# Kernel tuning notes

Hardware: AMD Instinct MI355X
Metric: run time of the kernel (lower is better)

The kernel has to match this reference:

```python
import jax, jax.numpy as jnp
import numpy as np

B, T, L = 16, 2048, 512
CH, H_ENC, H_DEC, ATTN_SZ, VOCAB, EMB = 256, 100, 200, 50, 6, 64


def _conv1d(x, k):
    # x: [B,T,Cin], k: [K,Cin,Cout], SAME padding, stride 1
    return jax.lax.conv_general_dilated(x, k, (1,), 'SAME', dimension_numbers=('NWC', 'WIO', 'NWC'))


def _lstm_step(x, c, h, W, b):
    # TF BasicLSTMCell: gates ordered [i, j, f, o], forget_bias = 1.0
    z = jnp.concatenate([x, h], -1) @ W + b
    i, j, f, o = jnp.split(z, 4, -1)
    nc = c * jax.nn.sigmoid(f + 1.0) + jax.nn.sigmoid(i) * jnp.tanh(j)
    nh = jnp.tanh(nc) * jax.nn.sigmoid(o)
    return nc, nh


def _run_lstm(xs, lengths, W, b, hidden):
    # dynamic_rnn semantics: beyond sequence_length, state held, output zeroed
    Bn, Tn, _ = xs.shape
    mask = (jnp.arange(Tn)[:, None] < lengths[None, :])[..., None]  # [T,B,1]

    def step(carry, inp):
        c, h = carry
        x, m = inp
        nc, nh = _lstm_step(x, c, h, W, b)
        c = jnp.where(m, nc, c)
        h = jnp.where(m, nh, h)
        return (c, h), jnp.where(m, nh, 0.0)

    init = (jnp.zeros((Bn, hidden), xs.dtype), jnp.zeros((Bn, hidden), xs.dtype))
    (c, h), outs = jax.lax.scan(step, init, (jnp.swapaxes(xs, 0, 1), mask))
    return jnp.swapaxes(outs, 0, 1), c, h


def _reverse_seq(x, lengths):
    # tf.reverse_sequence along time axis
    t = jnp.arange(x.shape[1])[None, :]
    idx = jnp.where(t < lengths[:, None], lengths[:, None] - 1 - t, t)
    return jnp.take_along_axis(x, idx[..., None], axis=1)


def setup_inputs():
    key = jax.random.key(0)
    ks = jax.random.split(key, 16)
    s = 0.05
    f32 = jnp.float32
    return {
        'signals': jax.random.normal(ks[0], (B, T), f32),
        'embeddings': jax.random.normal(ks[1], (VOCAB, EMB), f32) * s,
        'conv1_k': jax.random.normal(ks[2], (1, 1, CH), f32) * s,
        'conv1a_k': jax.random.normal(ks[3], (1, 1, CH), f32) * s,
        'conv1a_b': jnp.zeros((CH,), f32),
        'conv2_k': jax.random.normal(ks[4], (3, CH, CH), f32) * s,
        'conv3_k': jax.random.normal(ks[5], (1, CH, CH), f32) * s,
        'W_fwd': jax.random.normal(ks[6], (CH + H_ENC, 4 * H_ENC), f32) * s,
        'b_fwd': jnp.zeros((4 * H_ENC,), f32),
        'W_bwd': jax.random.normal(ks[7], (CH + H_ENC, 4 * H_ENC), f32) * s,
        'b_bwd': jnp.zeros((4 * H_ENC,), f32),
        'W_dec': jax.random.normal(ks[8], (EMB + ATTN_SZ + H_DEC, 4 * H_DEC), f32) * s,
        'b_dec': jnp.zeros((4 * H_DEC,), f32),
        'W_mem': jax.random.normal(ks[9], (H_DEC, H_DEC), f32) * s,
        'W_attn': jax.random.normal(ks[10], (2 * H_DEC, ATTN_SZ), f32) * s,
        'W_out': jax.random.normal(ks[11], (ATTN_SZ, VOCAB), f32) * s,
        'labels': jax.random.randint(ks[12], (B, L), 0, 4),
        'sig_length': jax.random.randint(ks[13], (B,), T // 2, T + 1),
        'base_length': jax.random.randint(ks[14], (B,), L // 2, L + 1),
    }


def reference(signals, embeddings, conv1_k, conv1a_k, conv1a_b, conv2_k, conv3_k,
              W_fwd, b_fwd, W_bwd, b_bwd, W_dec, b_dec, W_mem, W_attn, W_out,
              labels, sig_length, base_length):
    # ---- resBlock ----
    x = signals[..., None]                       # [B,T,1]
    c1 = _conv1d(x, conv1_k)                     # no bias
    c1a = _conv1d(x, conv1a_k) + conv1a_b        # with bias (shortcut)
    c3 = _conv1d(_conv1d(c1, conv2_k), conv3_k)
    feat = jax.nn.relu(c3 + c1a)                 # [B,T,256]

    # ---- bidirectional encoder ----
    fwd_out, cf, hf = _run_lstm(feat, sig_length, W_fwd, b_fwd, H_ENC)
    bwd_out, cb, hb = _run_lstm(_reverse_seq(feat, sig_length), sig_length, W_bwd, b_bwd, H_ENC)
    bwd_out = _reverse_seq(bwd_out, sig_length)
    memory = jnp.concatenate([fwd_out, bwd_out], -1)   # [B,T,200]
    c0 = jnp.concatenate([cf, cb], -1)                 # [B,200]
    h0 = jnp.concatenate([hf, hb], -1)

    # ---- Luong attention decoder (teacher forcing) ----
    keys = jnp.einsum('btd,de->bte', memory, W_mem)    # memory_layer (no bias)
    mem_mask = jnp.arange(T)[None, :] < sig_length[:, None]
    neg = jnp.finfo(memory.dtype).min
    emb = embeddings[labels]                            # [B,L,64]

    def dec_step(carry, x_t):
        c, h, attn = carry
        nc, nh = _lstm_step(jnp.concatenate([x_t, attn], -1), c, h, W_dec, b_dec)
        score = jnp.einsum('bd,btd->bt', nh, keys)
        align = jax.nn.softmax(jnp.where(mem_mask, score, neg), axis=-1)
        ctx = jnp.einsum('bt,btd->bd', align, memory)
        new_attn = jnp.concatenate([nh, ctx], -1) @ W_attn   # attention_layer (no bias)
        return (nc, nh, new_attn), new_attn @ W_out          # output Dense(6, no bias)

    attn0 = jnp.zeros((B, ATTN_SZ), memory.dtype)
    _, logits = jax.lax.scan(dec_step, (c0, h0, attn0), jnp.swapaxes(emb, 0, 1))
    logits = jnp.swapaxes(logits, 0, 1)                      # [B,L,6]
    dec_mask = (jnp.arange(L)[None, :] < base_length[:, None])[..., None]
    return jnp.where(dec_mask, logits, jnp.zeros((), logits.dtype))
```

## Files before the change

kernel.cpp:

```cpp
#include <hip/hip_runtime.h>

#define B_ 16
#define T_ 2048
#define L_ 512
#define HD 200
#define AT 50

__device__ __forceinline__ float rcp_(float x){ return __builtin_amdgcn_rcpf(x); }
__device__ __forceinline__ float sigf(float x){ return rcp_(1.f + __expf(-x)); }
__device__ __forceinline__ float tanhf_(float x){
  x = fminf(15.f, fmaxf(-15.f, x));
  float e = __expf(-2.f*x);
  return (1.f - e) * rcp_(1.f + e);
}
__device__ __forceinline__ unsigned bf16u(float v){
  unsigned u = __float_as_uint(v);
  u += 0x7FFFu + ((u >> 16) & 1u);
  return u >> 16;
}
__device__ __forceinline__ unsigned long long pkvs(float v, unsigned s){
  return (unsigned long long)__float_as_uint(v) | ((unsigned long long)s << 32);
}

__global__ void k_prep(const float* __restrict__ conv1, const float* __restrict__ conv1a,
                       const float* __restrict__ conv2, const float* __restrict__ conv3,
                       float* __restrict__ E)
{
  __shared__ float K2s[3*256];
  int tid = threadIdx.x;
  int k = tid >> 8, co = tid & 255;
  float a = 0.f;
  for (int ci = 0; ci < 256; ++ci)
    a = fmaf(conv1[ci], conv2[(k*256 + ci)*256 + co], a);
  K2s[k*256 + co] = a;
  __syncthreads();
  float b2 = 0.f;
  for (int ci = 0; ci < 256; ++ci)
    b2 = fmaf(K2s[k*256 + ci], conv3[ci*256 + co], b2);
  if (k == 1) b2 += conv1a[co];
  E[k*256 + co] = b2;
}

__global__ void k_feat(const float* __restrict__ sig, const float* __restrict__ E,
                       const float* __restrict__ c1ab, float* __restrict__ feat)
{
  int idx = blockIdx.x*256 + threadIdx.x;
  int row = idx >> 6;
  int c4  = (idx & 63) * 4;
  int t = row & (T_-1);
  float sm = (t > 0)     ? sig[row-1] : 0.f;
  float s0 = sig[row];
  float sp = (t < T_-1)  ? sig[row+1] : 0.f;
  float4 e0 = *(const float4*)&E[0*256 + c4];
  float4 e1 = *(const float4*)&E[1*256 + c4];
  float4 e2 = *(const float4*)&E[2*256 + c4];
  float4 bb = *(const float4*)&c1ab[c4];
  float4 r;
  r.x = fmaxf(0.f, fmaf(sm, e0.x, fmaf(s0, e1.x, fmaf(sp, e2.x, bb.x))));
  r.y = fmaxf(0.f, fmaf(sm, e0.y, fmaf(s0, e1.y, fmaf(sp, e2.y, bb.y))));
  r.z = fmaxf(0.f, fmaf(sm, e0.z, fmaf(s0, e1.z, fmaf(sp, e2.z, bb.z))));
  r.w = fmaxf(0.f, fmaf(sm, e0.w, fmaf(s0, e1.w, fmaf(sp, e2.w, bb.w))));
  *(float4*)&feat[(size_t)row*256 + c4] = r;
}

__global__ __launch_bounds__(256)
void k_gemm(const float* __restrict__ A, const float* __restrict__ B,
            const float* __restrict__ bias, float* __restrict__ C,
            int M, int N, int K, int ldb)
{
  __shared__ float As[16][132];
  __shared__ float Bs[16][68];
  int row0 = blockIdx.x*128, col0 = blockIdx.y*64;
  int tid = threadIdx.x;
  int tm = tid >> 4, tn = tid & 15;
  float acc[8][4] = {};
  for (int k0 = 0; k0 < K; k0 += 16){
    #pragma unroll
    for (int i = 0; i < 8; ++i){
      int e = tid + i*256;
      int m = e >> 4, kk = e & 15;
      float v = 0.f;
      if (k0 + kk < K) v = A[(size_t)(row0+m)*K + k0 + kk];
      As[kk][m] = v;
    }
    #pragma unroll
    for (int i = 0; i < 4; ++i){
      int e = tid + i*256;
      int n = e & 63, kb = e >> 6;
      float w = 0.f;
      if (k0 + kb < K && col0 + n < N) w = B[(size_t)(k0+kb)*ldb + col0 + n];
      Bs[kb][n] = w;
    }
    __syncthreads();
    #pragma unroll
    for (int kk = 0; kk < 16; ++kk){
      float a[8], bv[4];
      *(float4*)&a[0] = *(const float4*)&As[kk][tm*8];
      *(float4*)&a[4] = *(const float4*)&As[kk][tm*8+4];
      *(float4*)&bv[0] = *(const float4*)&Bs[kk][tn*4];
      #pragma unroll
      for (int i = 0; i < 8; ++i)
        #pragma unroll
        for (int j = 0; j < 4; ++j)
          acc[i][j] = fmaf(a[i], bv[j], acc[i][j]);
    }
    __syncthreads();
  }
  #pragma unroll
  for (int i = 0; i < 8; ++i){
    int r = row0 + tm*8 + i;
    #pragma unroll
    for (int j = 0; j < 4; ++j){
      int cc = col0 + tn*4 + j;
      if (cc < N) C[(size_t)r*N + cc] = acc[i][j] + (bias ? bias[cc] : 0.f);
    }
  }
}

__global__ void k_permW(const float* __restrict__ Wf, const float* __restrict__ bf,
                        const float* __restrict__ Wb, const float* __restrict__ bb,
                        float* __restrict__ WpF, float* __restrict__ WpB)
{
  int idx = blockIdx.x*256 + threadIdx.x;
  if (idx >= 2*357*400) return;
  int w = idx / (357*400), r = idx - w*(357*400);
  int j = r / 400, col = r - j*400;
  int src = (col & 3)*100 + (col >> 2);
  const float* W = w ? Wb : Wf; const float* bs = w ? bb : bf;
  float v = (j < 356) ? W[j*400 + src] : bs[src];
  (w ? WpB : WpF)[j*400 + col] = v;
}

__global__ __launch_bounds__(512, 1)
void k_encoder(const float* __restrict__ xprojF, const float* __restrict__ xprojB,
               const float* __restrict__ WpF, const float* __restrict__ WpB,
               const int* __restrict__ sig_len, float* __restrict__ memory,
               float* __restrict__ c0h0, int dirParam)
{
  int dir = dirParam, b = blockIdx.x;
  const float* xp = dir ? xprojB : xprojF;
  const float* Wp = dir ? WpB : WpF;
  int tid = threadIdx.x;
  bool act = tid < 400;
  int col = act ? tid : (tid - 400);
  int u = tid >> 2, gq = tid & 3;
  __shared__ __align__(16) float h2[2][104];
  float4 Uv[25];
  #pragma unroll
  for (int j4 = 0; j4 < 25; ++j4){
    Uv[j4].x = Wp[(256 + 4*j4 + 0)*400 + col];
    Uv[j4].y = Wp[(256 + 4*j4 + 1)*400 + col];
    Uv[j4].z = Wp[(256 + 4*j4 + 2)*400 + col];
    Uv[j4].w = Wp[(256 + 4*j4 + 3)*400 + col];
  }
  if (tid < 100) h2[0][tid] = 0.f;
  int len = sig_len[b];
  float c = 0.f, hfin = 0.f;
  int ta = dir ? (len-1) : 0;
  float xb0 = xp[((size_t)(b*T_ + ta))*400 + col];
  int tb_ = dir ? (len-2) : 1;
  float xb1 = xp[((size_t)(b*T_ + tb_))*400 + col];
  for (int step = 0; step < len; ++step){
    __syncthreads();
    int tn = dir ? (len-3-step) : (step+2);
    tn = tn < 0 ? 0 : (tn > T_-1 ? T_-1 : tn);
    float xn = xp[((size_t)(b*T_ + tn))*400 + col];
    const float* hb = h2[step & 1];
    float a0 = xb0, a1 = 0.f, a2 = 0.f, a3 = 0.f;
    #pragma unroll
    for (int j4 = 0; j4 < 25; ++j4){
      float4 h4 = *(const float4*)&hb[j4*4];
      a0 = fmaf(h4.x, Uv[j4].x, a0);
      a1 = fmaf(h4.y, Uv[j4].y, a1);
      a2 = fmaf(h4.z, Uv[j4].z, a2);
      a3 = fmaf(h4.w, Uv[j4].w, a3);
    }
    float z = (a0+a1)+(a2+a3);
    float v0 = z, v1 = __shfl_xor(z, 1);
    float v2 = __shfl_xor(v0, 2), v3 = __shfl_xor(v1, 2);
    float tA  = (gq&1) ? v1 : v0, tB  = (gq&1) ? v3 : v2;
    float tA2 = (gq&1) ? v0 : v1, tB2 = (gq&1) ? v2 : v3;
    float zi = (gq&2) ? tB  : tA;
    float zj = (gq&2) ? tB2 : tA2;
    float zf = (gq&2) ? tA  : tB;
    float zo = (gq&2) ? tA2 : tB2;
    c = c*sigf(zf + 1.f) + sigf(zi)*tanhf_(zj);
    float nh = tanhf_(c)*sigf(zo);
    hfin = nh;
    if (act && gq == 0){
      int t = dir ? (len-1-step) : step;
      h2[(step+1)&1][u] = nh;
      memory[((size_t)(b*T_ + t))*200 + dir*100 + u] = nh;
    }
    xb0 = xb1; xb1 = xn;
  }
  if (act && gq == 0){
    c0h0[b*400 + dir*100 + u]       = c;
    c0h0[b*400 + 200 + dir*100 + u] = hfin;
  }
  int total = (T_ - len)*100;
  for (int i = tid; i < total; i += 512){
    int t = len + i/100;
    int k = i - (i/100)*100;
    memory[((size_t)(b*T_ + t))*200 + dir*100 + k] = 0.f;
  }
}

__global__ void k_gather(const float* __restrict__ emb, const int* __restrict__ labels,
                         float* __restrict__ dA)
{
  int idx = blockIdx.x*256 + threadIdx.x;
  int i = idx >> 6, e = idx & 63;
  dA[(size_t)i*64 + e] = emb[labels[i]*64 + e];
}

__global__ void k_dec_init(unsigned long long* __restrict__ nhb,
                           unsigned long long* __restrict__ parts,
                           unsigned* __restrict__ flags, unsigned fval,
                           float* __restrict__ out)
{
  int idx = blockIdx.x*256 + threadIdx.x;
  if (idx < B_*L_*6) out[idx] = 0.f;
  if (idx < B_*HD) nhb[idx] = 0ull;
  if (idx < B_*16*112) parts[idx] = 0ull;
  if (idx < 32) flags[idx] = fval;
}

#define DEC_LDS 137728
#define TCH 128

__global__ __launch_bounds__(256, 1)
void k_fused(const float* __restrict__ xprojF, const float* __restrict__ xprojB,
             const float* __restrict__ WpF, const float* __restrict__ WpB,
             float* __restrict__ memG, float* c0h0,
             const float* __restrict__ W_mem, const float* __restrict__ W_attn,
             const float* __restrict__ decx, const float* __restrict__ W_dec,
             const float* __restrict__ W_out,
             const int* __restrict__ sig_len, const int* __restrict__ base_len,
             unsigned long long* nhb, unsigned long long* partials,
             unsigned* flags, int encInside,
             float* __restrict__ out)
{
  int blk = blockIdx.x;
  int b = (blk & 7) | (((blk >> 3) & 1) << 3);
  int g = blk >> 4;
  int tid = threadIdx.x;
  int u0 = g * 13;
  int nu = (HD - u0 < 13) ? (HD - u0) : 13;
  int t0 = g * TCH;

  extern __shared__ char smem[];
  uint2* keyP  = (uint2*)(smem);
  float* memAL = (float*)(smem + 51616);
  float* Uld   = (float*)(smem + 77216);
  float* Wa1s  = (float*)(smem + 129216);
  float* WoutL = (float*)(smem + 131824);
  float* nhF   = (float*)(smem + 133024);
  float* spL   = (float*)(smem + 133856);
  float* wL    = (float*)(smem + 134880);
  float* cpL   = (float*)(smem + 135392);
  float* apL   = (float*)(smem + 136016);
  float* zp    = (float*)(smem + 136224);
  float* attnL = (float*)(smem + 137056);
  float* SL    = (float*)(smem + 137264);
  float* ctxR  = (float*)(smem + 137272);
  float* apR   = (float*)(smem + 137480);

  if (encInside && g < 2){
    int dir = g;
    const float* xp = dir ? xprojB : xprojF;
    const float* Wp = dir ? WpB : WpF;
    float* h2 = spL;
    int col2 = (tid < 144) ? (256 + tid) : 256;
    float4 U1[25], U2[25];
    #pragma unroll
    for (int j4 = 0; j4 < 25; ++j4){
      U1[j4].x = Wp[(256 + 4*j4 + 0)*400 + tid];
      U1[j4].y = Wp[(256 + 4*j4 + 1)*400 + tid];
      U1[j4].z = Wp[(256 + 4*j4 + 2)*400 + tid];
      U1[j4].w = Wp[(256 + 4*j4 + 3)*400 + tid];
      U2[j4].x = Wp[(256 + 4*j4 + 0)*400 + col2];
      U2[j4].y = Wp[(256 + 4*j4 + 1)*400 + col2];
      U2[j4].z = Wp[(256 + 4*j4 + 2)*400 + col2];
      U2[j4].w = Wp[(256 + 4*j4 + 3)*400 + col2];
    }
    if (tid < 104) h2[tid] = 0.f;
    int len = sig_len[b];
    int u1 = tid >> 2, gq = tid & 3;
    int u2 = 64 + u1;
    float c1 = 0.f, c2 = 0.f, hf1 = 0.f, hf2 = 0.f;
    int taa = dir ? (len-1) : 0;
    int tbb = dir ? (len-2) : 1;
    float xA0 = xp[((size_t)(b*T_ + taa))*400 + tid];
    float xB0 = xp[((size_t)(b*T_ + taa))*400 + col2];
    float xA1 = xp[((size_t)(b*T_ + tbb))*400 + tid];
    float xB1 = xp[((size_t)(b*T_ + tbb))*400 + col2];
    for (int step = 0; step < len; ++step){
      __syncthreads();
      int tn = dir ? (len-3-step) : (step+2);
      tn = tn < 0 ? 0 : (tn > T_-1 ? T_-1 : tn);
      float xA2 = xp[((size_t)(b*T_ + tn))*400 + tid];
      float xB2 = xp[((size_t)(b*T_ + tn))*400 + col2];
      const float* hb = h2 + (step & 1)*104;
      float a0 = xA0, a1 = 0.f, a2 = 0.f, a3 = 0.f;
      float b0 = xB0, b1 = 0.f, b2 = 0.f, b3 = 0.f;
      #pragma unroll
      for (int j4 = 0; j4 < 25; ++j4){
        float4 h4 = *(const float4*)&hb[j4*4];
        a0 = fmaf(h4.x, U1[j4].x, a0);
        a1 = fmaf(h4.y, U1[j4].y, a1);
        a2 = fmaf(h4.z, U1[j4].z, a2);
        a3 = fmaf(h4.w, U1[j4].w, a3);
        b0 = fmaf(h4.x, U2[j4].x, b0);
        b1 = fmaf(h4.y, U2[j4].y, b1);
        b2 = fmaf(h4.z, U2[j4].z, b2);
        b3 = fmaf(h4.w, U2[j4].w, b3);
      }
      float z1 = (a0+a1)+(a2+a3);
      float z2 = (b0+b1)+(b2+b3);
      float v0 = z1, v1 = __shfl_xor(z1, 1);
      float v2 = __shfl_xor(v0, 2), v3 = __shfl_xor(v1, 2);
      float w0 = z2, w1 = __shfl_xor(z2, 1);
      float w2 = __shfl_xor(w0, 2), w3 = __shfl_xor(w1, 2);
      float tA, tB, tA2v, tB2v, zi, zj, zf, zo;
      tA  = (gq&1) ? v1 : v0; tB  = (gq&1) ? v3 : v2;
      tA2v = (gq&1) ? v0 : v1; tB2v = (gq&1) ? v2 : v3;
      zi = (gq&2) ? tB : tA;  zj = (gq&2) ? tB2v : tA2v;
      zf = (gq&2) ? tA : tB;  zo = (gq&2) ? tA2v : tB2v;
      c1 = c1*sigf(zf + 1.f) + sigf(zi)*tanhf_(zj);
      float nh1 = tanhf_(c1)*sigf(zo);
      hf1 = nh1;
      tA  = (gq&1) ? w1 : w0; tB  = (gq&1) ? w3 : w2;
      tA2v = (gq&1) ? w0 : w1; tB2v = (gq&1) ? w2 : w3;
      zi = (gq&2) ? tB : tA;  zj = (gq&2) ? tB2v : tA2v;
      zf = (gq&2) ? tA : tB;  zo = (gq&2) ? tA2v : tB2v;
      c2 = c2*sigf(zf + 1.f) + sigf(zi)*tanhf_(zj);
      float nh2 = tanhf_(c2)*sigf(zo);
      hf2 = nh2;
      float* hn = h2 + ((step+1)&1)*104;
      if (gq == 0){
        int t = dir ? (len-1-step) : step;
        hn[u1] = nh1;
        memG[((size_t)(b*T_ + t))*200 + dir*100 + u1] = nh1;
        if (tid < 144){
          hn[u2] = nh2;
          memG[((size_t)(b*T_ + t))*200 + dir*100 + u2] = nh2;
        }
      }
      xA0 = xA1; xA1 = xA2; xB0 = xB1; xB1 = xB2;
    }
    if ((tid & 3) == 0){
      int u1w = tid >> 2;
      c0h0[b*400 + dir*100 + u1w]       = c1;
      c0h0[b*400 + 200 + dir*100 + u1w] = hf1;
      if (tid < 144){
        c0h0[b*400 + dir*100 + 64 + u1w]       = c2;
        c0h0[b*400 + 200 + dir*100 + 64 + u1w] = hf2;
      }
    }
    int total = (T_ - len)*100;
    for (int i = tid; i < total; i += 256){
      int t = len + i/100;
      int k = i - (i/100)*100;
      memG[((size_t)(b*T_ + t))*200 + dir*100 + k] = 0.f;
    }
    __syncthreads();
    if (tid == 0){
      __builtin_amdgcn_fence(__ATOMIC_RELEASE, "agent");
      __hip_atomic_store(&flags[b*2 + dir], 1u,
                         __ATOMIC_RELAXED, __HIP_MEMORY_SCOPE_AGENT);
    }
  }

  if (encInside){
    if (tid == 0){
      while (__hip_atomic_load(&flags[b*2+0], __ATOMIC_RELAXED, __HIP_MEMORY_SCOPE_AGENT) == 0u)
        __builtin_amdgcn_s_sleep(8);
      while (__hip_atomic_load(&flags[b*2+1], __ATOMIC_RELAXED, __HIP_MEMORY_SCOPE_AGENT) == 0u)
        __builtin_amdgcn_s_sleep(8);
      __builtin_amdgcn_fence(__ATOMIC_ACQUIRE, "agent");
    }
    __syncthreads();
  }

  unsigned* stg = (unsigned*)Uld;
  for (int i = tid; i < TCH*100; i += 256){
    int t = i / 100, p2 = i - (i/100)*100;
    float2 mv = *(const float2*)&memG[((size_t)(b*T_ + t0 + t))*200 + 2*p2];
    stg[i] = bf16u(mv.x) | (bf16u(mv.y) << 16);
  }
  __syncthreads();
  {
    int t = tid >> 1, dh = tid & 1;
    const unsigned* mrow = stg + t*100;
    for (int dq = 0; dq < 25; ++dq){
      int d = dh*100 + dq*4;
      float ax = 0.f, ay = 0.f, az = 0.f, aw = 0.f;
      for (int p2 = 0; p2 < 100; ++p2){
        unsigned mm = mrow[p2];
        float m0 = __uint_as_float(mm << 16);
        float m1 = __uint_as_float(mm & 0xFFFF0000u);
        float4 w0 = *(const float4*)&W_mem[(size_t)(2*p2)*200 + d];
        float4 w1 = *(const float4*)&W_mem[(size_t)(2*p2+1)*200 + d];
        ax = fmaf(m0, w0.x, fmaf(m1, w1.x, ax));
        ay = fmaf(m0, w0.y, fmaf(m1, w1.y, ay));
        az = fmaf(m0, w0.z, fmaf(m1, w1.z, az));
        aw = fmaf(m0, w0.w, fmaf(m1, w1.w, aw));
      }
      keyP[(d>>2)*129 + t] = make_uint2(bf16u(ax) | (bf16u(ay) << 16),
                                        bf16u(az) | (bf16u(aw) << 16));
    }
    for (int dd = 0; dd < 25; ++dd){
      int d = dh*25 + dd;
      float acc = 0.f;
      for (int p2 = 0; p2 < 100; ++p2){
        unsigned mm = mrow[p2];
        float m0 = __uint_as_float(mm << 16);
        float m1 = __uint_as_float(mm & 0xFFFF0000u);
        acc = fmaf(m0, W_attn[(size_t)(200 + 2*p2)*50 + d],
              fmaf(m1, W_attn[(size_t)(201 + 2*p2)*50 + d], acc));
      }
      memAL[t*50 + d] = acc;
    }
  }
  __syncthreads();

  for (int i = tid; i < 250*52; i += 256){
    int j = i / 52, o_ = i - (i/52)*52;
    int uu = o_ >> 2, gg = o_ & 3;
    Uld[i] = (uu < nu) ? W_dec[(size_t)(64 + j)*800 + gg*200 + u0 + uu] : 0.f;
  }
  for (int i = tid; i < 13*50; i += 256){
    int uu = i / 50, d = i - (i/50)*50;
    Wa1s[i] = (uu < nu) ? W_attn[(size_t)(u0 + uu)*50 + d] : 0.f;
  }
  for (int i = tid; i < 300; i += 256) WoutL[i] = W_out[i];
  if (tid < 50) attnL[tid] = 0.f;
  if (tid < 8)  nhF[200 + tid] = 0.f;
  float creg = (tid < nu) ? c0h0[b*400 + u0 + tid] : 0.f;
  int len = sig_len[b];
  int Lb  = base_len[b];
  unsigned long long* nhB = nhb + (size_t)b*HD;
  __syncthreads();

  if (tid < 50) *(float4*)&nhF[tid*4] = *(const float4*)&c0h0[b*400 + 200 + tid*4];
  __syncthreads();
  int o  = tid - (tid/52)*52;
  int jc = tid / 52;
  float zh = 0.f, dcx = 0.f;
  if (tid < 208){
    const float* Ub = &Uld[(50 + jc*50)*52 + o];
    const float* hp = &nhF[jc*50];
    #pragma unroll 10
    for (int j = 0; j < 50; ++j) zh = fmaf(hp[j], Ub[(size_t)j*52], zh);
    if (jc == 0) dcx = decx[((size_t)(b*L_))*800 + (o&3)*200 + u0 + (o>>2)];
  }

  for (int l = 0; l < Lb; ++l){
    unsigned seq = (unsigned)(l + 1);
    if (tid < 208){
      float z = zh + ((jc == 0) ? dcx : 0.f);
      const float* Ub = &Uld[(jc*13)*52 + o];
      const float* ap_ = &attnL[jc*13];
      int cnt = (jc < 3) ? 13 : 11;
      for (int j = 0; j < cnt; ++j) z = fmaf(ap_[j], Ub[(size_t)j*52], z);
      zp[o*4 + jc] = z;
    } else if (g == 1 && l > 0 && tid < 214){
      int j = tid - 208;
      float o_ = 0.f;
      for (int d = 0; d < AT; ++d) o_ = fmaf(attnL[d], WoutL[d*6 + j], o_);
      out[((size_t)(b*L_ + (l-1)))*6 + j] = o_;
    }
    __syncthreads();
    if (tid < nu){
      const float* zz = &zp[(4*tid)*4];
      float zi = (zz[0]+zz[1])+(zz[2]+zz[3]);
      float zj = (zz[4]+zz[5])+(zz[6]+zz[7]);
      float zf = (zz[8]+zz[9])+(zz[10]+zz[11]);
      float zo = (zz[12]+zz[13])+(zz[14]+zz[15]);
      float c = creg;
      c = c*sigf(zf + 1.f) + sigf(zi)*tanhf_(zj);
      creg = c;
      float nh = tanhf_(c)*sigf(zo);
      __hip_atomic_store(&nhB[u0 + tid], pkvs(nh, seq),
                         __ATOMIC_RELAXED, __HIP_MEMORY_SCOPE_AGENT);
    }
    if (tid < HD){
      unsigned long long v;
      do {
        v = __hip_atomic_load(&nhB[tid], __ATOMIC_RELAXED, __HIP_MEMORY_SCOPE_AGENT);
      } while ((unsigned)(v >> 32) != seq);
      nhF[tid] = __uint_as_float((unsigned)v);
    }
    __syncthreads();
    {
      int t = tid & 127, dh = tid >> 7;
      const uint2* kp = &keyP[(dh*25)*129 + t];
      const float4* nf = (const float4*)nhF + dh*25;
      float s0 = 0.f, s1 = 0.f;
      #pragma unroll
      for (int q = 0; q < 25; ++q){
        uint2 kk = kp[(size_t)q*129];
        float4 nv = nf[q];
        s0 = fmaf(nv.x, __uint_as_float(kk.x << 16), s0);
        s1 = fmaf(nv.y, __uint_as_float(kk.x & 0xFFFF0000u), s1);
        s0 = fmaf(nv.z, __uint_as_float(kk.y << 16), s0);
        s1 = fmaf(nv.w, __uint_as_float(kk.y & 0xFFFF0000u), s1);
      }
      spL[tid] = s0 + s1;
    }
    __syncthreads();
    if (tid < 128){
      float s = spL[tid] + spL[tid + 128];
      float w = 0.f;
      if (t0 + tid < len){ s = fminf(60.f, fmaxf(-60.f, s)); w = __expf(s); }
      wL[tid] = w;
    } else if (tid < 178){
      int d = tid - 128;
      float a = 0.f;
      #pragma unroll
      for (int uu = 0; uu < 13; ++uu) a = fmaf(nhF[u0 + uu], Wa1s[uu*50 + d], a);
      apL[d] = a;
    }
    __syncthreads();
    if (tid >= 192){
      float v = wL[tid - 192] + wL[tid - 128];
      #pragma unroll
      for (int off = 32; off > 0; off >>= 1) v += __shfl_down(v, off);
      if (tid == 192) SL[0] = v;
    } else {
      int tc = tid >> 6, d = tid & 63;
      if (d < 50){
        int tlo = tc*43, thi = (tc == 2) ? 128 : tc*43 + 43;
        float a = 0.f;
        for (int t = tlo; t < thi; ++t) a = fmaf(wL[t], memAL[t*50 + d], a);
        cpL[tc*52 + d] = a;
      }
    }
    __syncthreads();
    {
      unsigned long long* pb = partials + (size_t)(b*16 + g)*112;
      if (tid < 50)
        __hip_atomic_store(&pb[tid],
                           pkvs((cpL[tid] + cpL[52 + tid]) + cpL[104 + tid], seq),
                           __ATOMIC_RELAXED, __HIP_MEMORY_SCOPE_AGENT);
      else if (tid < 100)
        __hip_atomic_store(&pb[tid], pkvs(apL[tid - 50], seq),
                           __ATOMIC_RELAXED, __HIP_MEMORY_SCOPE_AGENT);
      else if (tid == 100)
        __hip_atomic_store(&pb[100], pkvs(SL[0], seq),
                           __ATOMIC_RELAXED, __HIP_MEMORY_SCOPE_AGENT);
    }
    zh = 0.f;
    if (tid < 208){
      const float* Ub = &Uld[(50 + jc*50)*52 + o];
      const float* hp = &nhF[jc*50];
      #pragma unroll 10
      for (int j = 0; j < 50; ++j) zh = fmaf(hp[j], Ub[(size_t)j*52], zh);
      if (jc == 0 && l+1 < Lb)
        dcx = decx[((size_t)(b*L_ + (l+1)))*800 + (o&3)*200 + u0 + (o>>2)];
    }
    if (tid < 101){
      const unsigned long long* base = partials + (size_t)b*16*112 + tid;
      unsigned long long v[16];
      #pragma unroll
      for (int gg = 0; gg < 16; ++gg)
        v[gg] = __hip_atomic_load(&base[gg*112], __ATOMIC_RELAXED, __HIP_MEMORY_SCOPE_AGENT);
      #pragma unroll
      for (int gg = 0; gg < 16; ++gg)
        while ((unsigned)(v[gg] >> 32) != seq)
          v[gg] = __hip_atomic_load(&base[gg*112], __ATOMIC_RELAXED, __HIP_MEMORY_SCOPE_AGENT);
      float acc = 0.f;
      #pragma unroll
      for (int gg = 0; gg < 16; ++gg) acc += __uint_as_float((unsigned)v[gg]);
      if (tid < 50) ctxR[tid] = acc;
      else if (tid < 100) apR[tid - 50] = acc;
      else SL[1] = acc;
    }
    __syncthreads();
    if (tid < 50) attnL[tid] = fmaf(ctxR[tid], rcp_(SL[1]), apR[tid]);
    __syncthreads();
  }
  if (g == 1 && tid < 6){
    float o_ = 0.f;
    for (int d = 0; d < AT; ++d) o_ = fmaf(attnL[d], WoutL[d*6 + tid], o_);
    out[((size_t)(b*L_ + (Lb-1)))*6 + tid] = o_;
  }
}

extern "C" void kernel_launch(void* const* d_in, const int* in_sizes, int n_in,
                              void* d_out, int out_size, void* d_ws, size_t ws_size,
                              hipStream_t stream)
{
  const float* signals   = (const float*)d_in[0];
  const float* embeddings= (const float*)d_in[1];
  const float* conv1_k   = (const float*)d_in[2];
  const float* conv1a_k  = (const float*)d_in[3];
  const float* conv1a_b  = (const float*)d_in[4];
  const float* conv2_k   = (const float*)d_in[5];
  const float* conv3_k   = (const float*)d_in[6];
  const float* W_fwd     = (const float*)d_in[7];
  const float* b_fwd     = (const float*)d_in[8];
  const float* W_bwd     = (const float*)d_in[9];
  const float* b_bwd     = (const float*)d_in[10];
  const float* W_dec     = (const float*)d_in[11];
  const float* b_dec     = (const float*)d_in[12];
  const float* W_mem     = (const float*)d_in[13];
  const float* W_attn    = (const float*)d_in[14];
  const float* W_out     = (const float*)d_in[15];
  const int*   labels    = (const int*)d_in[16];
  const int*   sig_len   = (const int*)d_in[17];
  const int*   base_len  = (const int*)d_in[18];
  float* out = (float*)d_out;
  char* ws = (char*)d_ws;

  const size_t o_c0h0     = 4096;
  const size_t o_nhbuf    = 32768;
  const size_t o_partials = 65536;
  const size_t o_flags    = 458752;
  const size_t o_WpF      = 589824;
  const size_t o_WpB      = 1161024;
  const size_t o_feat     = 4194304;
  const size_t o_mem      = o_feat + 33554432;
  const size_t o_X1       = o_mem + 26214400;
  const size_t o_X2       = o_X1 + 52428800;

  bool bigws = (ws_size >= o_X2 + 52428800);

  float* E      = (float*)(ws);
  float* c0h0   = (float*)(ws + o_c0h0);
  unsigned long long* nhbuf = (unsigned long long*)(ws + o_nhbuf);
  unsigned long long* parts = (unsigned long long*)(ws + o_partials);
  unsigned* flags = (unsigned*)(ws + o_flags);
  float* WpF    = (float*)(ws + o_WpF);
  float* WpB    = (float*)(ws + o_WpB);
  float* feat   = (float*)(ws + o_feat);
  float* memory = (float*)(ws + o_mem);
  float* xprojF = (float*)(ws + o_X1);
  float* xprojB = bigws ? (float*)(ws + o_X2) : xprojF;
  float* decxA  = (float*)(ws + o_feat);
  float* decx   = (float*)(ws + o_feat + 4194304);

  k_prep<<<1, 768, 0, stream>>>(conv1_k, conv1a_k, conv2_k, conv3_k, E);
  k_feat<<<8192, 256, 0, stream>>>(signals, E, conv1a_b, feat);
  k_permW<<<1116, 256, 0, stream>>>(W_fwd, b_fwd, W_bwd, b_bwd, WpF, WpB);

  dim3 gx(256, 7);
  if (bigws){
    k_gemm<<<gx, 256, 0, stream>>>(feat, WpF, WpF + 356*400, xprojF, 32768, 400, 256, 400);
    k_gemm<<<gx, 256, 0, stream>>>(feat, WpB, WpB + 356*400, xprojB, 32768, 400, 256, 400);
  } else {
    k_gemm<<<gx, 256, 0, stream>>>(feat, WpF, WpF + 356*400, xprojF, 32768, 400, 256, 400);
    k_encoder<<<16, 512, 0, stream>>>(xprojF, xprojF, WpF, WpB, sig_len, memory, c0h0, 0);
    k_gemm<<<gx, 256, 0, stream>>>(feat, WpB, WpB + 356*400, xprojF, 32768, 400, 256, 400);
    k_encoder<<<16, 512, 0, stream>>>(xprojF, xprojF, WpF, WpB, sig_len, memory, c0h0, 1);
  }

  k_gather<<<2048, 256, 0, stream>>>(embeddings, labels, decxA);
  k_gemm<<<dim3(64, 13), 256, 0, stream>>>(decxA, W_dec, b_dec, decx, 8192, 800, 64, 800);
  k_dec_init<<<192, 256, 0, stream>>>(nhbuf, parts, flags, bigws ? 0u : 1u, out);

  hipFuncSetAttribute(reinterpret_cast<const void*>(k_fused),
                      hipFuncAttributeMaxDynamicSharedMemorySize, DEC_LDS);
  k_fused<<<256, 256, DEC_LDS, stream>>>(xprojF, xprojB, WpF, WpB,
                                         memory, c0h0, W_mem, W_attn,
                                         decx, W_dec, W_out,
                                         sig_len, base_len,
                                         nhbuf, parts, flags, bigws ? 1 : 0,
                                         out);
}
```

Measured before the change: 5.110 ms.

## Double fused kernel block size to 512 threads and repartition per-step work

Launches the fused encoder/decoder kernel with 512 threads instead of 256. The encoder LSTM assigns one gate column per thread instead of two, and the decoder splits the recurrent h-projection into 8 chunks and the score and context reductions into more partitions. This shortens the serial per-thread work on each recurrent step, which lies on the critical path. In exchange it uses more LDS, may raise register pressure, adds an extra barrier and reduction step, and the encoder has a few idle threads.

```diff
diff --git a/kernel.cpp b/kernel.cpp
--- a/kernel.cpp
+++ b/kernel.cpp
@@ -226,10 +226,10 @@
   if (idx < 32) flags[idx] = fval;
 }
 
-#define DEC_LDS 137728
+#define DEC_LDS 141440
 #define TCH 128
 
-__global__ __launch_bounds__(256, 1)
+__global__ __launch_bounds__(512, 1)
 void k_fused(const float* __restrict__ xprojF, const float* __restrict__ xprojB,
              const float* __restrict__ WpF, const float* __restrict__ WpB,
              float* __restrict__ memG, float* c0h0,
@@ -257,109 +257,79 @@
   float* WoutL = (float*)(smem + 131824);
   float* nhF   = (float*)(smem + 133024);
   float* spL   = (float*)(smem + 133856);
-  float* wL    = (float*)(smem + 134880);
-  float* cpL   = (float*)(smem + 135392);
-  float* apL   = (float*)(smem + 136016);
-  float* zp    = (float*)(smem + 136224);
-  float* attnL = (float*)(smem + 137056);
-  float* SL    = (float*)(smem + 137264);
-  float* ctxR  = (float*)(smem + 137272);
-  float* apR   = (float*)(smem + 137480);
+  float* wL    = (float*)(smem + 135904);
+  float* cpL   = (float*)(smem + 136416);
+  float* apL   = (float*)(smem + 138080);
+  float* zp8   = (float*)(smem + 138288);
+  float* zpA   = (float*)(smem + 139952);
+  float* attnL = (float*)(smem + 140784);
+  float* SL    = (float*)(smem + 140992);
+  float* ctxR  = (float*)(smem + 141000);
+  float* apR   = (float*)(smem + 141208);
 
   if (encInside && g < 2){
     int dir = g;
     const float* xp = dir ? xprojB : xprojF;
     const float* Wp = dir ? WpB : WpF;
     float* h2 = spL;
-    int col2 = (tid < 144) ? (256 + tid) : 256;
-    float4 U1[25], U2[25];
+    bool act = tid < 400;
+    int col = act ? tid : (tid - 400);
+    int u = tid >> 2, gq = tid & 3;
+    float4 Uv[25];
     #pragma unroll
     for (int j4 = 0; j4 < 25; ++j4){
-      U1[j4].x = Wp[(256 + 4*j4 + 0)*400 + tid];
-      U1[j4].y = Wp[(256 + 4*j4 + 1)*400 + tid];
-      U1[j4].z = Wp[(256 + 4*j4 + 2)*400 + tid];
-      U1[j4].w = Wp[(256 + 4*j4 + 3)*400 + tid];
-      U2[j4].x = Wp[(256 + 4*j4 + 0)*400 + col2];
-      U2[j4].y = Wp[(256 + 4*j4 + 1)*400 + col2];
-      U2[j4].z = Wp[(256 + 4*j4 + 2)*400 + col2];
-      U2[j4].w = Wp[(256 + 4*j4 + 3)*400 + col2];
-    }
-    if (tid < 104) h2[tid] = 0.f;
+      Uv[j4].x = Wp[(256 + 4*j4 + 0)*400 + col];
+      Uv[j4].y = Wp[(256 + 4*j4 + 1)*400 + col];
+      Uv[j4].z = Wp[(256 + 4*j4 + 2)*400 + col];
+      Uv[j4].w = Wp[(256 + 4*j4 + 3)*400 + col];
+    }
+    if (tid < 104) { h2[tid] = 0.f; h2[104 + tid] = 0.f; }
     int len = sig_len[b];
-    int u1 = tid >> 2, gq = tid & 3;
-    int u2 = 64 + u1;
-    float c1 = 0.f, c2 = 0.f, hf1 = 0.f, hf2 = 0.f;
-    int taa = dir ? (len-1) : 0;
-    int tbb = dir ? (len-2) : 1;
-    float xA0 = xp[((size_t)(b*T_ + taa))*400 + tid];
-    float xB0 = xp[((size_t)(b*T_ + taa))*400 + col2];
-    float xA1 = xp[((size_t)(b*T_ + tbb))*400 + tid];
-    float xB1 = xp[((size_t)(b*T_ + tbb))*400 + col2];
+    float c = 0.f, hfin = 0.f;
+    int ta = dir ? (len-1) : 0;
+    float xb0 = xp[((size_t)(b*T_ + ta))*400 + col];
+    int tb_ = dir ? (len-2) : 1;
+    float xb1 = xp[((size_t)(b*T_ + tb_))*400 + col];
     for (int step = 0; step < len; ++step){
       __syncthreads();
       int tn = dir ? (len-3-step) : (step+2);
       tn = tn < 0 ? 0 : (tn > T_-1 ? T_-1 : tn);
-      float xA2 = xp[((size_t)(b*T_ + tn))*400 + tid];
-      float xB2 = xp[((size_t)(b*T_ + tn))*400 + col2];
+      float xn = xp[((size_t)(b*T_ + tn))*400 + col];
       const float* hb = h2 + (step & 1)*104;
-      float a0 = xA0, a1 = 0.f, a2 = 0.f, a3 = 0.f;
-      float b0 = xB0, b1 = 0.f, b2 = 0.f, b3 = 0.f;
+      float a0 = xb0, a1 = 0.f, a2 = 0.f, a3 = 0.f;
       #pragma unroll
       for (int j4 = 0; j4 < 25; ++j4){
         float4 h4 = *(const float4*)&hb[j4*4];
-        a0 = fmaf(h4.x, U1[j4].x, a0);
-        a1 = fmaf(h4.y, U1[j4].y, a1);
-        a2 = fmaf(h4.z, U1[j4].z, a2);
-        a3 = fmaf(h4.w, U1[j4].w, a3);
-        b0 = fmaf(h4.x, U2[j4].x, b0);
-        b1 = fmaf(h4.y, U2[j4].y, b1);
-        b2 = fmaf(h4.z, U2[j4].z, b2);
-        b3 = fmaf(h4.w, U2[j4].w, b3);
+        a0 = fmaf(h4.x, Uv[j4].x, a0);
+        a1 = fmaf(h4.y, Uv[j4].y, a1);
+        a2 = fmaf(h4.z, Uv[j4].z, a2);
+        a3 = fmaf(h4.w, Uv[j4].w, a3);
       }
-      float z1 = (a0+a1)+(a2+a3);
-      float z2 = (b0+b1)+(b2+b3);
-      float v0 = z1, v1 = __shfl_xor(z1, 1);
+      float z = (a0+a1)+(a2+a3);
+      float v0 = z, v1 = __shfl_xor(z, 1);
       float v2 = __shfl_xor(v0, 2), v3 = __shfl_xor(v1, 2);
-      float w0 = z2, w1 = __shfl_xor(z2, 1);
-      float w2 = __shfl_xor(w0, 2), w3 = __shfl_xor(w1, 2);
-      float tA, tB, tA2v, tB2v, zi, zj, zf, zo;
-      tA  = (gq&1) ? v1 : v0; tB  = (gq&1) ? v3 : v2;
-      tA2v = (gq&1) ? v0 : v1; tB2v = (gq&1) ? v2 : v3;
-      zi = (gq&2) ? tB : tA;  zj = (gq&2) ? tB2v : tA2v;
-      zf = (gq&2) ? tA : tB;  zo = (gq&2) ? tA2v : tB2v;
-      c1 = c1*sigf(zf + 1.f) + sigf(zi)*tanhf_(zj);
-      float nh1 = tanhf_(c1)*sigf(zo);
-      hf1 = nh1;
-      tA  = (gq&1) ? w1 : w0; tB  = (gq&1) ? w3 : w2;
-      tA2v = (gq&1) ? w0 : w1; tB2v = (gq&1) ? w2 : w3;
-      zi = (gq&2) ? tB : tA;  zj = (gq&2) ? tB2v : tA2v;
-      zf = (gq&2) ? tA : tB;  zo = (gq&2) ? tA2v : tB2v;
-      c2 = c2*sigf(zf + 1.f) + sigf(zi)*tanhf_(zj);
-      float nh2 = tanhf_(c2)*sigf(zo);
-      hf2 = nh2;
-      float* hn = h2 + ((step+1)&1)*104;
-      if (gq == 0){
+      float tA  = (gq&1) ? v1 : v0, tB  = (gq&1) ? v3 : v2;
+      float tA2 = (gq&1) ? v0 : v1, tB2 = (gq&1) ? v2 : v3;
+      float zi = (gq&2) ? tB  : tA;
+      float zj = (gq&2) ? tB2 : tA2;
+      float zf = (gq&2) ? tA  : tB;
+      float zo = (gq&2) ? tA2 : tB2;
+      c = c*sigf(zf + 1.f) + sigf(zi)*tanhf_(zj);
+      float nh = tanhf_(c)*sigf(zo);
+      hfin = nh;
+      if (act && gq == 0){
         int t = dir ? (len-1-step) : step;
-        hn[u1] = nh1;
-        memG[((size_t)(b*T_ + t))*200 + dir*100 + u1] = nh1;
-        if (tid < 144){
-          hn[u2] = nh2;
-          memG[((size_t)(b*T_ + t))*200 + dir*100 + u2] = nh2;
-        }
+        h2[((step+1)&1)*104 + u] = nh;
+        memG[((size_t)(b*T_ + t))*200 + dir*100 + u] = nh;
       }
-      xA0 = xA1; xA1 = xA2; xB0 = xB1; xB1 = xB2;
-    }
-    if ((tid & 3) == 0){
-      int u1w = tid >> 2;
-      c0h0[b*400 + dir*100 + u1w]       = c1;
-      c0h0[b*400 + 200 + dir*100 + u1w] = hf1;
-      if (tid < 144){
-        c0h0[b*400 + dir*100 + 64 + u1w]       = c2;
-        c0h0[b*400 + 200 + dir*100 + 64 + u1w] = hf2;
-      }
+      xb0 = xb1; xb1 = xn;
+    }
+    if (act && gq == 0){
+      c0h0[b*400 + dir*100 + u]       = c;
+      c0h0[b*400 + 200 + dir*100 + u] = hfin;
     }
     int total = (T_ - len)*100;
-    for (int i = tid; i < total; i += 256){
+    for (int i = tid; i < total; i += 512){
       int t = len + i/100;
       int k = i - (i/100)*100;
       memG[((size_t)(b*T_ + t))*200 + dir*100 + k] = 0.f;
@@ -384,58 +354,57 @@
   }
 
   unsigned* stg = (unsigned*)Uld;
-  for (int i = tid; i < TCH*100; i += 256){
+  for (int i = tid; i < TCH*100; i += 512){
     int t = i / 100, p2 = i - (i/100)*100;
     float2 mv = *(const float2*)&memG[((size_t)(b*T_ + t0 + t))*200 + 2*p2];
     stg[i] = bf16u(mv.x) | (bf16u(mv.y) << 16);
   }
   __syncthreads();
-  {
-    int t = tid >> 1, dh = tid & 1;
+  for (int i = tid; i < TCH*50; i += 512){
+    int t = i / 50, q = i - (i/50)*50;
+    int d = q*4;
     const unsigned* mrow = stg + t*100;
-    for (int dq = 0; dq < 25; ++dq){
-      int d = dh*100 + dq*4;
-      float ax = 0.f, ay = 0.f, az = 0.f, aw = 0.f;
-      for (int p2 = 0; p2 < 100; ++p2){
-        unsigned mm = mrow[p2];
-        float m0 = __uint_as_float(mm << 16);
-        float m1 = __uint_as_float(mm & 0xFFFF0000u);
-        float4 w0 = *(const float4*)&W_mem[(size_t)(2*p2)*200 + d];
-        float4 w1 = *(const float4*)&W_mem[(size_t)(2*p2+1)*200 + d];
-        ax = fmaf(m0, w0.x, fmaf(m1, w1.x, ax));
-        ay = fmaf(m0, w0.y, fmaf(m1, w1.y, ay));
-        az = fmaf(m0, w0.z, fmaf(m1, w1.z, az));
-        aw = fmaf(m0, w0.w, fmaf(m1, w1.w, aw));
-      }
-      keyP[(d>>2)*129 + t] = make_uint2(bf16u(ax) | (bf16u(ay) << 16),
-                                        bf16u(az) | (bf16u(aw) << 16));
-    }
-    for (int dd = 0; dd < 25; ++dd){
-      int d = dh*25 + dd;
-      float acc = 0.f;
-      for (int p2 = 0; p2 < 100; ++p2){
-        unsigned mm = mrow[p2];
-        float m0 = __uint_as_float(mm << 16);
-        float m1 = __uint_as_float(mm & 0xFFFF0000u);
-        acc = fmaf(m0, W_attn[(size_t)(200 + 2*p2)*50 + d],
-              fmaf(m1, W_attn[(size_t)(201 + 2*p2)*50 + d], acc));
-      }
-      memAL[t*50 + d] = acc;
-    }
+    float ax = 0.f, ay = 0.f, az = 0.f, aw = 0.f;
+    for (int p2 = 0; p2 < 100; ++p2){
+      unsigned mm = mrow[p2];
+      float m0 = __uint_as_float(mm << 16);
+      float m1 = __uint_as_float(mm & 0xFFFF0000u);
+      float4 w0 = *(const float4*)&W_mem[(size_t)(2*p2)*200 + d];
+      float4 w1 = *(const float4*)&W_mem[(size_t)(2*p2+1)*200 + d];
+      ax = fmaf(m0, w0.x, fmaf(m1, w1.x, ax));
+      ay = fmaf(m0, w0.y, fmaf(m1, w1.y, ay));
+      az = fmaf(m0, w0.z, fmaf(m1, w1.z, az));
+      aw = fmaf(m0, w0.w, fmaf(m1, w1.w, aw));
+    }
+    keyP[q*129 + t] = make_uint2(bf16u(ax) | (bf16u(ay) << 16),
+                                 bf16u(az) | (bf16u(aw) << 16));
+  }
+  for (int i = tid; i < TCH*50; i += 512){
+    int t = i / 50, d = i - (i/50)*50;
+    const unsigned* mrow = stg + t*100;
+    float acc = 0.f;
+    for (int p2 = 0; p2 < 100; ++p2){
+      unsigned mm = mrow[p2];
+      float m0 = __uint_as_float(mm << 16);
+      float m1 = __uint_as_float(mm & 0xFFFF0000u);
+      acc = fmaf(m0, W_attn[(size_t)(200 + 2*p2)*50 + d],
+            fmaf(m1, W_attn[(size_t)(201 + 2*p2)*50 + d], acc));
+    }
+    memAL[t*50 + d] = acc;
   }
   __syncthreads();
 
-  for (int i = tid; i < 250*52; i += 256){
+  for (int i = tid; i < 250*52; i += 512){
     int j = i / 52, o_ = i - (i/52)*52;
     int uu = o_ >> 2, gg = o_ & 3;
     Uld[i] = (uu < nu) ? W_dec[(size_t)(64 + j)*800 + gg*200 + u0 + uu] : 0.f;
   }
-  for (int i = tid; i < 13*50; i += 256){
-    int uu = i / 50, d = i - (i/50)*50;
-    Wa1s[i] = (uu < nu) ? W_attn[(size_t)(u0 + uu)*50 + d] : 0.f;
-  }
-  for (int i = tid; i < 300; i += 256) WoutL[i] = W_out[i];
-  if (tid < 50) attnL[tid] = 0.f;
+  for (int i = tid; i < 13*50; i += 512){
+    int uw = i / 50, d = i - (i/50)*50;
+    Wa1s[i] = (uw < nu) ? W_attn[(size_t)(u0 + uw)*50 + d] : 0.f;
+  }
+  for (int i = tid; i < 300; i += 512) WoutL[i] = W_out[i];
+  if (tid < 52) attnL[tid] = 0.f;
   if (tid < 8)  nhF[200 + tid] = 0.f;
   float creg = (tid < nu) ? c0h0[b*400 + u0 + tid] : 0.f;
   int len = sig_len[b];
@@ -446,26 +415,30 @@
   if (tid < 50) *(float4*)&nhF[tid*4] = *(const float4*)&c0h0[b*400 + 200 + tid*4];
   __syncthreads();
   int o  = tid - (tid/52)*52;
-  int jc = tid / 52;
-  float zh = 0.f, dcx = 0.f;
-  if (tid < 208){
-    const float* Ub = &Uld[(50 + jc*50)*52 + o];
-    const float* hp = &nhF[jc*50];
-    #pragma unroll 10
-    for (int j = 0; j < 50; ++j) zh = fmaf(hp[j], Ub[(size_t)j*52], zh);
-    if (jc == 0) dcx = decx[((size_t)(b*L_))*800 + (o&3)*200 + u0 + (o>>2)];
-  }
+  int jc8 = tid / 52;
+  int jc4 = tid / 52;
+  float dcx = 0.f;
+  if (tid < 416){
+    const float* Ub = &Uld[(50 + jc8*25)*52 + o];
+    const float* hp = &nhF[jc8*25];
+    float zh = 0.f;
+    #pragma unroll
+    for (int j = 0; j < 25; ++j) zh = fmaf(hp[j], Ub[(size_t)j*52], zh);
+    zp8[o*8 + jc8] = zh;
+    if (tid < 52) dcx = decx[((size_t)(b*L_))*800 + (o&3)*200 + u0 + (o>>2)];
+  }
+  __syncthreads();
 
   for (int l = 0; l < Lb; ++l){
     unsigned seq = (unsigned)(l + 1);
     if (tid < 208){
-      float z = zh + ((jc == 0) ? dcx : 0.f);
-      const float* Ub = &Uld[(jc*13)*52 + o];
-      const float* ap_ = &attnL[jc*13];
-      int cnt = (jc < 3) ? 13 : 11;
+      float z = zp8[o*8 + 2*jc4] + zp8[o*8 + 2*jc4 + 1] + ((jc4 == 0) ? dcx : 0.f);
+      const float* Ub = &Uld[(jc4*13)*52 + o];
+      const float* ap_ = &attnL[jc4*13];
+      int cnt = (jc4 < 3) ? 13 : 11;
       for (int j = 0; j < cnt; ++j) z = fmaf(ap_[j], Ub[(size_t)j*52], z);
-      zp[o*4 + jc] = z;
-    } else if (g == 1 && l > 0 && tid < 214){
+      zpA[o*4 + jc4] = z;
+    } else if (g == 1 && l > 0 && tid >= 208 && tid < 214){
       int j = tid - 208;
       float o_ = 0.f;
       for (int d = 0; d < AT; ++d) o_ = fmaf(attnL[d], WoutL[d*6 + j], o_);
@@ -473,7 +446,7 @@
     }
     __syncthreads();
     if (tid < nu){
-      const float* zz = &zp[(4*tid)*4];
+      const float* zz = &zpA[16*tid];
       float zi = (zz[0]+zz[1])+(zz[2]+zz[3]);
       float zj = (zz[4]+zz[5])+(zz[6]+zz[7]);
       float zf = (zz[8]+zz[9])+(zz[10]+zz[11]);
@@ -495,11 +468,12 @@
     __syncthreads();
     {
       int t = tid & 127, dh = tid >> 7;
-      const uint2* kp = &keyP[(dh*25)*129 + t];
-      const float4* nf = (const float4*)nhF + dh*25;
+      int pstart = (dh < 2) ? dh*13 : 26 + (dh-2)*12;
+      int pcnt   = (dh < 2) ? 13 : 12;
+      const uint2* kp = &keyP[pstart*129 + t];
+      const float4* nf = (const float4*)nhF + pstart;
       float s0 = 0.f, s1 = 0.f;
-      #pragma unroll
-      for (int q = 0; q < 25; ++q){
+      for (int q = 0; q < pcnt; ++q){
         uint2 kk = kp[(size_t)q*129];
         float4 nv = nf[q];
         s0 = fmaf(nv.x, __uint_as_float(kk.x << 16), s0);
@@ -511,7 +485,7 @@
     }
     __syncthreads();
     if (tid < 128){
-      float s = spL[tid] + spL[tid + 128];
+      float s = (spL[tid] + spL[tid + 128]) + (spL[tid + 256] + spL[tid + 384]);
       float w = 0.f;
       if (t0 + tid < len){ s = fminf(60.f, fmaxf(-60.f, s)); w = __expf(s); }
       wL[tid] = w;
@@ -519,19 +493,19 @@
       int d = tid - 128;
       float a = 0.f;
       #pragma unroll
-      for (int uu = 0; uu < 13; ++uu) a = fmaf(nhF[u0 + uu], Wa1s[uu*50 + d], a);
+      for (int uw = 0; uw < 13; ++uw) a = fmaf(nhF[u0 + uw], Wa1s[uw*50 + d], a);
       apL[d] = a;
     }
     __syncthreads();
-    if (tid >= 192){
-      float v = wL[tid - 192] + wL[tid - 128];
+    if (tid >= 448){
+      float v = wL[tid - 448] + wL[tid - 384];
       #pragma unroll
       for (int off = 32; off > 0; off >>= 1) v += __shfl_down(v, off);
-      if (tid == 192) SL[0] = v;
+      if (tid == 448) SL[0] = v;
     } else {
       int tc = tid >> 6, d = tid & 63;
       if (d < 50){
-        int tlo = tc*43, thi = (tc == 2) ? 128 : tc*43 + 43;
+        int tlo = tc*18, thi = (tc == 6) ? 128 : tlo + 18;
         float a = 0.f;
         for (int t = tlo; t < thi; ++t) a = fmaf(wL[t], memAL[t*50 + d], a);
         cpL[tc*52 + d] = a;
@@ -540,39 +514,42 @@
     __syncthreads();
     {
       unsigned long long* pb = partials + (size_t)(b*16 + g)*112;
-      if (tid < 50)
-        __hip_atomic_store(&pb[tid],
-                           pkvs((cpL[tid] + cpL[52 + tid]) + cpL[104 + tid], seq),
+      if (tid < 50){
+        float p0 = 0.f;
+        #pragma unroll
+        for (int k = 0; k < 7; ++k) p0 += cpL[k*52 + tid];
+        __hip_atomic_store(&pb[tid], pkvs(p0, seq),
                            __ATOMIC_RELAXED, __HIP_MEMORY_SCOPE_AGENT);
-      else if (tid < 100)
+      } else if (tid < 100)
         __hip_atomic_store(&pb[tid], pkvs(apL[tid - 50], seq),
                            __ATOMIC_RELAXED, __HIP_MEMORY_SCOPE_AGENT);
       else if (tid == 100)
         __hip_atomic_store(&pb[100], pkvs(SL[0], seq),
                            __ATOMIC_RELAXED, __HIP_MEMORY_SCOPE_AGENT);
     }
-    zh = 0.f;
-    if (tid < 208){
-      const float* Ub = &Uld[(50 + jc*50)*52 + o];
-      const float* hp = &nhF[jc*50];
-      #pragma unroll 10
-      for (int j = 0; j < 50; ++j) zh = fmaf(hp[j], Ub[(size_t)j*52], zh);
-      if (jc == 0 && l+1 < Lb)
+    if (tid < 416){
+      const float* Ub = &Uld[(50 + jc8*25)*52 + o];
+      const float* hp = &nhF[jc8*25];
+      float zh = 0.f;
+      #pragma unroll
+      for (int j = 0; j < 25; ++j) zh = fmaf(hp[j], Ub[(size_t)j*52], zh);
+      zp8[o*8 + jc8] = zh;
+      if (tid < 52 && l+1 < Lb)
         dcx = decx[((size_t)(b*L_ + (l+1)))*800 + (o&3)*200 + u0 + (o>>2)];
     }
     if (tid < 101){
       const unsigned long long* base = partials + (size_t)b*16*112 + tid;
       unsigned long long v[16];
       #pragma unroll
-      for (int gg = 0; gg < 16; ++gg)
-        v[gg] = __hip_atomic_load(&base[gg*112], __ATOMIC_RELAXED, __HIP_MEMORY_SCOPE_AGENT);
-      #pragma unroll
-      for (int gg = 0; gg < 16; ++gg)
-        while ((unsigned)(v[gg] >> 32) != seq)
-          v[gg] = __hip_atomic_load(&base[gg*112], __ATOMIC_RELAXED, __HIP_MEMORY_SCOPE_AGENT);
+      for (int gq2 = 0; gq2 < 16; ++gq2)
+        v[gq2] = __hip_atomic_load(&base[gq2*112], __ATOMIC_RELAXED, __HIP_MEMORY_SCOPE_AGENT);
+      #pragma unroll
+      for (int gq2 = 0; gq2 < 16; ++gq2)
+        while ((unsigned)(v[gq2] >> 32) != seq)
+          v[gq2] = __hip_atomic_load(&base[gq2*112], __ATOMIC_RELAXED, __HIP_MEMORY_SCOPE_AGENT);
       float acc = 0.f;
       #pragma unroll
-      for (int gg = 0; gg < 16; ++gg) acc += __uint_as_float((unsigned)v[gg]);
+      for (int gq2 = 0; gq2 < 16; ++gq2) acc += __uint_as_float((unsigned)v[gq2]);
       if (tid < 50) ctxR[tid] = acc;
       else if (tid < 100) apR[tid - 50] = acc;
       else SL[1] = acc;
@@ -662,7 +639,7 @@
 
   hipFuncSetAttribute(reinterpret_cast<const void*>(k_fused),
                       hipFuncAttributeMaxDynamicSharedMemorySize, DEC_LDS);
-  k_fused<<<256, 256, DEC_LDS, stream>>>(xprojF, xprojB, WpF, WpB,
+  k_fused<<<256, 512, DEC_LDS, stream>>>(xprojF, xprojB, WpF, WpB,
                                          memory, c0h0, W_mem, W_attn,
                                          decx, W_dec, W_out,
                                          sig_len, base_len,
```

Result: faster. 4.348 ms (-14.9%).
